# Performance work log

Hardware: AMD Instinct MI355X
Metric: run time of the kernel (lower is better)

## Reference

```python
import jax, jax.numpy as jnp
import numpy as np

XYZ_MIN = jnp.array([-1.0, -1.0, -1.0], dtype=jnp.float32)
XYZ_MAX = jnp.array([1.0, 1.0, 1.0], dtype=jnp.float32)
ALPHA_INIT = 0.01
ACT_SHIFT = float(np.log(1.0 / (1.0 - ALPHA_INIT) - 1.0))
INTERVAL = 0.5  # stepsize * voxel_size_ratio
NEAR, FAR = 0.2, 1.8
N_RAYS, N_SAMPLES = 4096, 256
GRID = 160
K0_DIM = 12
VIEW_PE = 4
WIDTH = 128
DIM0 = 3 + 3 * VIEW_PE * 2 + K0_DIM  # 39


def trilinear(grid, pts):
    """grid: [X,Y,Z,C]; pts: [N,3] world coords -> [N,C] (align_corners=True, border clamp)."""
    sz = jnp.array(grid.shape[:3], dtype=pts.dtype)
    ijk = (pts - XYZ_MIN) / (XYZ_MAX - XYZ_MIN) * (sz - 1.0)
    ijk = jnp.clip(ijk, 0.0, sz - 1.0)
    lo = jnp.clip(jnp.floor(ijk).astype(jnp.int32), 0, jnp.array(grid.shape[:3], jnp.int32) - 2)
    f = ijk - lo.astype(pts.dtype)
    hi = lo + 1
    x0, y0, z0 = lo[:, 0], lo[:, 1], lo[:, 2]
    x1, y1, z1 = hi[:, 0], hi[:, 1], hi[:, 2]
    fx, fy, fz = f[:, 0:1], f[:, 1:2], f[:, 2:3]
    c00 = grid[x0, y0, z0] * (1 - fz) + grid[x0, y0, z1] * fz
    c01 = grid[x0, y1, z0] * (1 - fz) + grid[x0, y1, z1] * fz
    c10 = grid[x1, y0, z0] * (1 - fz) + grid[x1, y0, z1] * fz
    c11 = grid[x1, y1, z0] * (1 - fz) + grid[x1, y1, z1] * fz
    c0 = c00 * (1 - fy) + c01 * fy
    c1 = c10 * (1 - fy) + c11 * fy
    return c0 * (1 - fx) + c1 * fx


def setup_inputs() -> dict:
    key = jax.random.key(0)
    ks = jax.random.split(key, 8)
    rays_o = jax.random.uniform(ks[0], (N_RAYS, 3), jnp.float32, -0.3, 0.3)
    rays_d = jax.random.normal(ks[1], (N_RAYS, 3), jnp.float32)
    density = jax.random.normal(ks[2], (GRID, GRID, GRID), jnp.float32)
    k0 = jax.random.normal(ks[3], (K0_DIM, GRID, GRID, GRID), jnp.float32) * 0.1
    W0 = jax.random.normal(ks[4], (DIM0, WIDTH), jnp.float32) * (1.0 / np.sqrt(DIM0))
    b0 = jnp.zeros((WIDTH,), jnp.float32)
    W1 = jax.random.normal(ks[5], (WIDTH, WIDTH), jnp.float32) * (1.0 / np.sqrt(WIDTH))
    b1 = jnp.zeros((WIDTH,), jnp.float32)
    W2 = jax.random.normal(ks[6], (WIDTH, 3), jnp.float32) * (1.0 / np.sqrt(WIDTH))
    b2 = jnp.zeros((3,), jnp.float32)
    return {"rays_o": rays_o, "rays_d": rays_d, "density": density, "k0": k0,
            "W0": W0, "b0": b0, "W1": W1, "b1": b1, "W2": W2, "b2": b2}


def reference(rays_o, rays_d, density, k0, W0, b0, W1, b1, W2, b2):
    R, S = rays_o.shape[0], N_SAMPLES
    viewdirs = rays_d / jnp.linalg.norm(rays_d, axis=-1, keepdims=True)
    t = jnp.linspace(NEAR, FAR, S, dtype=rays_o.dtype)  # [S]
    pts = rays_o[:, None, :] + rays_d[:, None, :] * t[None, :, None]  # [R,S,3]
    ptsf = pts.reshape(-1, 3)

    # Raw2Alpha: alpha = 1 - (1 + exp(d + shift))^(-interval)
    sigma = trilinear(density[..., None], ptsf)[:, 0].reshape(R, S)
    alpha = 1.0 - jnp.power(1.0 + jnp.exp(sigma + ACT_SHIFT), -INTERVAL)

    # Alphas2Weights: per-ray exclusive cumprod of transmittance
    Tcum = jnp.cumprod(1.0 - alpha + 1e-10, axis=1)  # [R,S]
    T = jnp.concatenate([jnp.ones((R, 1), alpha.dtype), Tcum[:, :-1]], axis=1)
    weights = alpha * T
    alphainv_last = Tcum[:, -1]

    # k0 features + view positional encoding -> rgbnet MLP
    feat = trilinear(jnp.moveaxis(k0, 0, -1), ptsf).reshape(R, S, K0_DIM)
    freq = (2.0 ** jnp.arange(VIEW_PE)).astype(rays_o.dtype)  # [P]
    vf = viewdirs[:, :, None] * freq[None, None, :]  # [R,3,P]
    vemb = jnp.concatenate([viewdirs, jnp.sin(vf).reshape(R, -1), jnp.cos(vf).reshape(R, -1)], axis=-1)  # [R,27]
    x = jnp.concatenate([feat, jnp.broadcast_to(vemb[:, None, :], (R, S, vemb.shape[-1]))], axis=-1)  # [R,S,39]

    h = jax.nn.relu(x @ W0 + b0)
    h = jax.nn.relu(h @ W1 + b1)
    rgb = jax.nn.sigmoid(h @ W2 + b2)  # [R,S,3]

    # composite with white background
    rgb_marched = jnp.sum(weights[..., None] * rgb, axis=1) + alphainv_last[:, None]
    return rgb_marched
```

## Files before the change

### kernel.cpp

```cpp
#include <hip/hip_runtime.h>
#include <hip/hip_bf16.h>

#define NRAYS 4096
#define NS 256
#define G 160
#define G2 (160*160)
#define G3 (160*160*160)
#define K0DIM 12
#define WIDTH 128
#define CHUNK 16
#define NCHUNK 16
#define HBS 136
#define ACT_SHIFT_F (-4.5951198501345889f)
#define TNEAR 0.2f
#define TFAR 1.8f

#define WS_W1G_OFF 1024
#define WS_W0G_OFF (1024 + 32768)
#define WS_PACK_OFF 65536
#define PACK_BYTES ((size_t)G3 * 16 * 2)
#define WS_NEED_AOS ((size_t)WS_PACK_OFF + PACK_BYTES)

typedef unsigned short u16;
typedef unsigned int u32;
typedef __attribute__((ext_vector_type(8))) short short8;
typedef __attribute__((ext_vector_type(4))) float floatx4;

#define W1F_IDX(kq, qs, n) (((((kq)<<2) + (qs)) * 128 + (n)) << 3)

__device__ __forceinline__ float bf2f(u16 u) {
    union { u32 i; float f; } v; v.i = ((u32)u) << 16; return v.f;
}
__device__ __forceinline__ u16 f2bf(float f) {
    union { float f; u32 u; } v; v.f = f;
    u32 r = v.u + 0x7FFFu + ((v.u >> 16) & 1u);
    return (u16)(r >> 16);
}

__device__ __forceinline__ float loadv(const float* p, int i) { return p[i]; }
__device__ __forceinline__ float loadv(const u16* p, int i)   { return bf2f(p[i]); }
__device__ __forceinline__ void storev(float* p, int i, float v) { p[i] = v; }
__device__ __forceinline__ void storev(u16* p, int i, float v)   { p[i] = f2bf(v); }
__device__ __forceinline__ float tofl(float v) { return v; }
__device__ __forceinline__ float tofl(u16 v)   { return bf2f(v); }
__device__ __forceinline__ float ldm(const void* p, int i, int mode) {
    return mode ? ((const float*)p)[i] : bf2f(((const u16*)p)[i]);
}

struct Coords { int base; float fx, fy, fz; };

__device__ __forceinline__ Coords coords_n(float px, float py, float pz) {
    float gx = fminf(fmaxf((px + 1.0f) * 79.5f, 0.0f), 159.0f);
    float gy = fminf(fmaxf((py + 1.0f) * 79.5f, 0.0f), 159.0f);
    float gz = fminf(fmaxf((pz + 1.0f) * 79.5f, 0.0f), 159.0f);
    int ix = (int)gx; if (ix > 158) ix = 158;
    int iy = (int)gy; if (iy > 158) iy = 158;
    int iz = (int)gz; if (iz > 158) iz = 158;
    Coords c;
    c.base = (ix * G + iy) * G + iz;
    c.fx = gx - (float)ix; c.fy = gy - (float)iy; c.fz = gz - (float)iz;
    return c;
}

__global__ void decide_mode(const u16* __restrict__ rays_d_u16, int* __restrict__ mode) {
    __shared__ int cnt;
    if (threadIdx.x == 0) cnt = 0;
    __syncthreads();
    if (threadIdx.x < 128) {
        u16 u = rays_d_u16[threadIdx.x];
        int e = (u >> 7) & 0xFF;
        int m = u & 0x7F;
        float v = bf2f(u);
        if (e == 0xFF || (e == 0 && m != 0) || fabsf(v) > 32.0f) atomicAdd(&cnt, 1);
    }
    __syncthreads();
    if (threadIdx.x == 0) *mode = (cnt >= 4) ? 1 : 0;
}

__global__ void pack_weights(const void* __restrict__ W1, const void* __restrict__ W0,
                             u16* __restrict__ w1g, u16* __restrict__ w0g,
                             const int* __restrict__ mode) {
    const int m = *mode;
    const int idx = blockIdx.x * 256 + threadIdx.x;
    for (int i = idx; i < WIDTH * WIDTH; i += 64 * 256) {
        int k = i >> 7, n = i & 127;
        float v = m ? ((const float*)W1)[i] : bf2f(((const u16*)W1)[i]);
        w1g[W1F_IDX(k >> 5, (k >> 3) & 3, n) + (k & 7)] = f2bf(v);
    }
    for (int i = idx; i < WIDTH * 16; i += 64 * 256) {
        int n = i >> 4, k = i & 15;
        float v = 0.0f;
        if (k < K0DIM) v = m ? ((const float*)W0)[k * WIDTH + n] : bf2f(((const u16*)W0)[k * WIDTH + n]);
        w0g[i] = f2bf(v);
    }
}

__global__ __launch_bounds__(256)
void repack_grid(const void* __restrict__ density, const void* __restrict__ k0,
                 u16* __restrict__ packed, const int* __restrict__ modep) {
    const int mode = *modep;
    const u32 vox = (u32)blockIdx.x * 128u + (u32)(threadIdx.x & 127);
    const int h = threadIdx.x >> 7;
    u16 o[8];
    if (mode) {
        const float* kf = (const float*)k0;
        const float* df = (const float*)density;
        if (h == 0) {
            #pragma unroll
            for (int c = 0; c < 8; c++) o[c] = f2bf(kf[(size_t)c*G3 + vox]);
        } else {
            #pragma unroll
            for (int c = 0; c < 4; c++) o[c] = f2bf(kf[(size_t)(8+c)*G3 + vox]);
            o[4] = f2bf(df[vox]); o[5] = 0; o[6] = 0; o[7] = 0;
        }
    } else {
        const u16* ku = (const u16*)k0;
        const u16* du = (const u16*)density;
        if (h == 0) {
            #pragma unroll
            for (int c = 0; c < 8; c++) o[c] = ku[(size_t)c*G3 + vox];
        } else {
            #pragma unroll
            for (int c = 0; c < 4; c++) o[c] = ku[(size_t)(8+c)*G3 + vox];
            o[4] = du[vox]; o[5] = 0; o[6] = 0; o[7] = 0;
        }
    }
    short8 ov;
    #pragma unroll
    for (int j = 0; j < 8; j++) ov[j] = (short)o[j];
    *(short8*)(packed + (size_t)vox*16 + (size_t)h*8) = ov;
}

__global__ __launch_bounds__(256, 4)
void dvgo_aos(const void* __restrict__ rays_o, const void* __restrict__ rays_d,
              const void* __restrict__ W0, const void* __restrict__ b0,
              const void* __restrict__ b1, const void* __restrict__ W2,
              const void* __restrict__ b2,
              const u16* __restrict__ packed, const u16* __restrict__ w1g,
              const u16* __restrict__ w0g, void* __restrict__ out,
              const int* __restrict__ modep)
{
    const int mode = *modep;

    __shared__ __align__(16) u16   featB[64 * 16];
    __shared__ __align__(16) u16   h0B[16 * HBS];
    __shared__ __align__(16) u16   h1B[16 * HBS];
    __shared__ float p2[4 * 16 * 12];
    __shared__ float rgbs[NS * 3];
    __shared__ float wts[NS];
    __shared__ float base0[WIDTH];
    __shared__ float vembs[27];
    __shared__ float ainvs;

    const int r = blockIdx.x;
    const int tid = threadIdx.x;

    const float o0 = ldm(rays_o, r*3+0, mode);
    const float o1 = ldm(rays_o, r*3+1, mode);
    const float o2 = ldm(rays_o, r*3+2, mode);
    const float d0 = ldm(rays_d, r*3+0, mode);
    const float d1 = ldm(rays_d, r*3+1, mode);
    const float d2 = ldm(rays_d, r*3+2, mode);

    const int lane = tid & 63;
    const int wvid = tid >> 6;
    const int q    = lane >> 4;
    const int ncol = lane & 15;
    const int col0 = wvid*32 + ncol;
    const int col1 = col0 + 16;

    const int sm  = tid >> 2;
    const int gdy = tid & 1;
    const int gdx = (tid >> 1) & 1;
    const u32 coff = (u32)(gdx*G2 + gdy*G) * 16u;

    float gfx, gfy, gfz;
    short8 qg[4];

    #define ISSUE_G(C0N) do {                                                     \
        float tv_ = TNEAR + (TFAR-TNEAR)*((float)((C0N)+sm) * (1.0f/255.0f));     \
        Coords ce_ = coords_n(o0+d0*tv_, o1+d1*tv_, o2+d2*tv_);                   \
        gfx = ce_.fx; gfy = ce_.fy; gfz = ce_.fz;                                 \
        const u16* g_ = packed + ((u32)ce_.base*16u + coff);                      \
        qg[0] = *(const short8*)(g_);                                             \
        qg[1] = *(const short8*)(g_ + 8);                                         \
        qg[2] = *(const short8*)(g_ + 16);                                        \
        qg[3] = *(const short8*)(g_ + 24);                                        \
    } while(0)

    #define COMMIT_G(C0N) do {                                                    \
        float wxy_ = (gdx ? gfx : 1.0f-gfx) * (gdy ? gfy : 1.0f-gfy);             \
        float v_[13];                                                             \
        _Pragma("unroll")                                                         \
        for (int c_ = 0; c_ < 8; c_++) {                                          \
            float lo_ = bf2f((u16)qg[0][c_]);                                     \
            float hi_ = bf2f((u16)qg[2][c_]);                                     \
            v_[c_] = (lo_ + gfz*(hi_-lo_)) * wxy_;                                \
        }                                                                         \
        _Pragma("unroll")                                                         \
        for (int c_ = 0; c_ < 5; c_++) {                                          \
            float lo_ = bf2f((u16)qg[1][c_]);                                     \
            float hi_ = bf2f((u16)qg[3][c_]);                                     \
            v_[8+c_] = (lo_ + gfz*(hi_-lo_)) * wxy_;                              \
        }                                                                         \
        _Pragma("unroll")                                                         \
        for (int c_ = 0; c_ < 13; c_++) {                                         \
            v_[c_] += __shfl_xor(v_[c_], 1, 64);                                  \
            v_[c_] += __shfl_xor(v_[c_], 2, 64);                                  \
        }                                                                         \
        if ((tid & 3) == 0) {                                                     \
            _Pragma("unroll")                                                     \
            for (int c_ = 0; c_ < 6; c_++) {                                      \
                u32 pk_ = (u32)f2bf(v_[2*c_]) | ((u32)f2bf(v_[2*c_+1]) << 16);    \
                *(u32*)&featB[sm*16 + 2*c_] = pk_;                                \
            }                                                                     \
            float alpha_ = 1.0f - rsqrtf(1.0f + __expf(v_[12] + ACT_SHIFT_F));    \
            wts[(C0N) + sm] = alpha_;                                             \
        }                                                                         \
    } while(0)

    ISSUE_G(0);

    short8 w1r[4][2];
    #pragma unroll
    for (int kq = 0; kq < 4; kq++) {
        w1r[kq][0] = *(const short8*)&w1g[W1F_IDX(kq, q, col0)];
        w1r[kq][1] = *(const short8*)&w1g[W1F_IDX(kq, q, col1)];
    }
    short8 w0r0 = {}, w0r1 = {};
    if (q < 2) {
        w0r0 = *(const short8*)&w0g[(col0 << 4) + q*8];
        w0r1 = *(const short8*)&w0g[(col1 << 4) + q*8];
    }
    short8 w2r;
    #pragma unroll
    for (int j = 0; j < 8; j++) {
        u16 t_ = 0;
        if (ncol < 3) t_ = f2bf(ldm(W2, (wvid*32 + q*8 + j)*3 + ncol, mode));
        w2r[j] = (short)t_;
    }
    const float b2v = (ncol < 3) ? ldm(b2, ncol, mode) : 0.0f;
    const float b1c0 = ldm(b1, col0, mode);
    const float b1c1 = ldm(b1, col1, mode);

    for (int i = tid; i < 64*4; i += 256)
        featB[(i >> 2)*16 + 12 + (i & 3)] = 0;

    if (tid < 27) {
        float inv = rsqrtf(d0*d0 + d1*d1 + d2*d2);
        float v0 = d0*inv, v1 = d1*inv, v2 = d2*inv;
        float val;
        if (tid < 3) {
            val = (tid == 0) ? v0 : ((tid == 1) ? v1 : v2);
        } else if (tid < 15) {
            int t2 = tid - 3; int dd = t2 >> 2; int p = t2 & 3;
            float vd = (dd == 0) ? v0 : ((dd == 1) ? v1 : v2);
            val = sinf(vd * (float)(1 << p));
        } else {
            int t2 = tid - 15; int dd = t2 >> 2; int p = t2 & 3;
            float vd = (dd == 0) ? v0 : ((dd == 1) ? v1 : v2);
            val = cosf(vd * (float)(1 << p));
        }
        vembs[tid] = val;
    }
    __syncthreads();

    if (tid < WIDTH) {
        float a = ldm(b0, tid, mode);
        #pragma unroll
        for (int i = 0; i < 27; i++)
            a += vembs[i] * ldm(W0, (K0DIM + i)*WIDTH + tid, mode);
        base0[tid] = a;
    }
    __syncthreads();

    const float bs00 = base0[col0], bs01 = base0[col1];

    for (int mi = 0; mi < 4; mi++) {
        COMMIT_G(mi*64);
        if (mi < 3) ISSUE_G((mi+1)*64);
        __syncthreads();

        for (int ti = 0; ti < 4; ti++) {
            short8 af0 = (short8){0,0,0,0,0,0,0,0};
            if (q < 2) af0 = *(const short8*)&featB[(ti*16 + ncol)*16 + q*8];
            floatx4 a0 = (floatx4){bs00,bs00,bs00,bs00};
            floatx4 a1 = (floatx4){bs01,bs01,bs01,bs01};
            a0 = __builtin_amdgcn_mfma_f32_16x16x32_bf16(af0, w0r0, a0, 0, 0, 0);
            a1 = __builtin_amdgcn_mfma_f32_16x16x32_bf16(af0, w0r1, a1, 0, 0, 0);
            #pragma unroll
            for (int rI = 0; rI < 4; rI++) {
                h0B[(q*4+rI)*HBS + col0] = f2bf(fmaxf(a0[rI], 0.0f));
                h0B[(q*4+rI)*HBS + col1] = f2bf(fmaxf(a1[rI], 0.0f));
            }
            __syncthreads();

            floatx4 c0a = (floatx4){b1c0,b1c0,b1c0,b1c0};
            floatx4 c1a = (floatx4){b1c1,b1c1,b1c1,b1c1};
            #pragma unroll
            for (int kq = 0; kq < 4; kq++) {
                short8 af = *(const short8*)&h0B[ncol*HBS + kq*32 + q*8];
                c0a = __builtin_amdgcn_mfma_f32_16x16x32_bf16(af, w1r[kq][0], c0a, 0, 0, 0);
                c1a = __builtin_amdgcn_mfma_f32_16x16x32_bf16(af, w1r[kq][1], c1a, 0, 0, 0);
            }
            #pragma unroll
            for (int rI = 0; rI < 4; rI++) {
                h1B[(q*4+rI)*HBS + col0] = f2bf(fmaxf(c0a[rI], 0.0f));
                h1B[(q*4+rI)*HBS + col1] = f2bf(fmaxf(c1a[rI], 0.0f));
            }
            __syncthreads();

            short8 af2 = *(const short8*)&h1B[ncol*HBS + wvid*32 + q*8];
            floatx4 pp = (floatx4){0.0f,0.0f,0.0f,0.0f};
            if (wvid == 0 && ncol < 3) pp = (floatx4){b2v,b2v,b2v,b2v};
            pp = __builtin_amdgcn_mfma_f32_16x16x32_bf16(af2, w2r, pp, 0, 0, 0);
            if (ncol < 3) {
                #pragma unroll
                for (int rI = 0; rI < 4; rI++)
                    p2[ti*192 + (q*4+rI)*12 + wvid*3 + ncol] = pp[rI];
            }
            __syncthreads();

            if (tid < 48) {
                int c_ = tid >> 4, s_ = tid & 15;
                int pb = ti*192 + s_*12;
                float x = p2[pb + c_] + p2[pb + 3 + c_] + p2[pb + 6 + c_] + p2[pb + 9 + c_];
                rgbs[(mi*64 + ti*16 + s_)*3 + c_] = 1.0f / (1.0f + __expf(-x));
            }
        }
    }

    __syncthreads();

    if (tid < 64) {
        const int l = tid;
        float a0 = wts[4*l+0], a1 = wts[4*l+1], a2 = wts[4*l+2], a3 = wts[4*l+3];
        float m0 = 1.0f - a0 + 1e-10f;
        float m1 = 1.0f - a1 + 1e-10f;
        float m2 = 1.0f - a2 + 1e-10f;
        float m3 = 1.0f - a3 + 1e-10f;
        float sc = (m0*m1)*(m2*m3);
        #pragma unroll
        for (int dlt = 1; dlt < 64; dlt <<= 1) {
            float o = __shfl_up(sc, dlt, 64);
            if (l >= dlt) sc *= o;
        }
        float Tr = __shfl_up(sc, 1, 64);
        if (l == 0) Tr = 1.0f;
        wts[4*l+0] = a0 * Tr; Tr *= m0;
        wts[4*l+1] = a1 * Tr; Tr *= m1;
        wts[4*l+2] = a2 * Tr; Tr *= m2;
        wts[4*l+3] = a3 * Tr; Tr *= m3;
        if (l == 63) ainvs = Tr;
    }
    __syncthreads();

    if (wvid < 3) {
        float a = 0.0f;
        #pragma unroll
        for (int j = 0; j < 4; j++) {
            int s = lane*4 + j;
            a += wts[s] * rgbs[s*3 + wvid];
        }
        #pragma unroll
        for (int m = 1; m <= 32; m <<= 1) a += __shfl_xor(a, m, 64);
        if (lane == 0) {
            float v = a + ainvs;
            if (mode) ((float*)out)[r*3 + wvid] = v;
            else      ((u16*)out)[r*3 + wvid]   = f2bf(v);
        }
    }
    #undef ISSUE_G
    #undef COMMIT_G
}

template <typename T, typename OT, int MODE>
__global__ __launch_bounds__(256, 4)
void dvgo_fb(const T* __restrict__ rays_o, const T* __restrict__ rays_d,
             const T* __restrict__ density, const T* __restrict__ k0,
             const T* __restrict__ W0, const T* __restrict__ b0,
             const T* __restrict__ W1, const T* __restrict__ b1,
             const T* __restrict__ W2, const T* __restrict__ b2,
             const u16* __restrict__ w1g, const u16* __restrict__ w0g,
             OT* __restrict__ out, const int* __restrict__ mode)
{
    if (*mode != MODE) return;

    __shared__ __align__(16) u16   h0B[CHUNK * HBS];
    __shared__ __align__(16) u16   featB[CHUNK * 16];
    __shared__ __align__(16) float W2Tf[3 * WIDTH];
    __shared__ float p2[CHUNK * 12];
    __shared__ float base0[WIDTH];
    __shared__ float b1s[WIDTH];
    __shared__ float b2s[3];
    __shared__ float vembs[27];
    __shared__ float wts[NS];
    __shared__ float red[48];
    __shared__ float ainvs;

    const int r = blockIdx.x;
    const int tid = threadIdx.x;

    const float o0 = loadv(rays_o, r*3+0);
    const float o1 = loadv(rays_o, r*3+1);
    const float o2 = loadv(rays_o, r*3+2);
    const float d0 = loadv(rays_d, r*3+0);
    const float d1 = loadv(rays_d, r*3+1);
    const float d2 = loadv(rays_d, r*3+2);

    const int lane = tid & 63;
    const int wvid = tid >> 6;
    const int q    = lane >> 4;
    const int ncol = lane & 15;
    const int col0 = wvid*32 + ncol;
    const int col1 = col0 + 16;

    T areg[8]; float afx, afy, afz;
    {
        float tv = TNEAR + (TFAR - TNEAR) * ((float)tid * (1.0f/(float)(NS-1)));
        Coords c = coords_n(o0 + d0*tv, o1 + d1*tv, o2 + d2*tv);
        afx = c.fx; afy = c.fy; afz = c.fz;
        const T* g = density + (u32)c.base;
        areg[0]=g[0]; areg[1]=g[1]; areg[2]=g[G]; areg[3]=g[G+1];
        areg[4]=g[G2]; areg[5]=g[G2+1]; areg[6]=g[G2+G]; areg[7]=g[G2+G+1];
    }

    short8 w1r[4][2];
    #pragma unroll
    for (int kq = 0; kq < 4; kq++) {
        w1r[kq][0] = *(const short8*)&w1g[W1F_IDX(kq, q, col0)];
        w1r[kq][1] = *(const short8*)&w1g[W1F_IDX(kq, q, col1)];
    }
    short8 w0r0 = {}, w0r1 = {};
    if (q < 2) {
        w0r0 = *(const short8*)&w0g[(col0 << 4) + q*8];
        w0r1 = *(const short8*)&w0g[(col1 << 4) + q*8];
    }

    const int gch = tid >> 4;
    const int gs  = tid & 15;
    const bool gact = (gch < K0DIM);
    const T* gbase = k0 + (size_t)(gact ? gch : 0) * G3;

    #define ISSUE(C0N, Q, FX, FY, FZ) do { if (gact) {                          \
        float tv_ = TNEAR + (TFAR-TNEAR)*((float)((C0N)+gs) * (1.0f/255.0f));   \
        Coords ce_ = coords_n(o0+d0*tv_, o1+d1*tv_, o2+d2*tv_);                 \
        FX = ce_.fx; FY = ce_.fy; FZ = ce_.fz;                                  \
        const T* g_ = gbase + (u32)ce_.base;                                    \
        Q[0]=g_[0]; Q[1]=g_[1]; Q[2]=g_[G]; Q[3]=g_[G+1];                       \
        Q[4]=g_[G2]; Q[5]=g_[G2+1]; Q[6]=g_[G2+G]; Q[7]=g_[G2+G+1];             \
    } } while(0)

    #define COMMIT(Q, FX, FY, FZ) do { if (gact) {                              \
        float z0_=tofl(Q[0]), z1_=tofl(Q[1]), z2_=tofl(Q[2]), z3_=tofl(Q[3]);   \
        float z4_=tofl(Q[4]), z5_=tofl(Q[5]), z6_=tofl(Q[6]), z7_=tofl(Q[7]);   \
        float c00_ = z0_ + (FZ)*(z1_-z0_);                                      \
        float c01_ = z2_ + (FZ)*(z3_-z2_);                                      \
        float c10_ = z4_ + (FZ)*(z5_-z4_);                                      \
        float c11_ = z6_ + (FZ)*(z7_-z6_);                                      \
        float e0_ = c00_ + (FY)*(c01_-c00_);                                    \
        float e1_ = c10_ + (FY)*(c11_-c10_);                                    \
        featB[gs*16 + gch] = f2bf(e0_ + (FX)*(e1_-e0_));                        \
    } } while(0)

    T qa[8], qn[8];
    float fxa, fya, fza, fxn, fyn, fzn;
    ISSUE(0, qa, fxa, fya, fza);
    ISSUE(CHUNK, qn, fxn, fyn, fzn);

    for (int i = tid; i < CHUNK*4; i += 256)
        featB[(i >> 2)*16 + 12 + (i & 3)] = 0;
    for (int k = tid; k < 3*WIDTH; k += 256) {
        int c = k >> 7, i = k & 127;
        W2Tf[k] = loadv(W2, i*3 + c);
    }
    if (tid < WIDTH) b1s[tid] = loadv(b1, tid);
    if (tid < 3)     b2s[tid] = loadv(b2, tid);

    if (tid < 27) {
        float inv = rsqrtf(d0*d0 + d1*d1 + d2*d2);
        float v0 = d0*inv, v1 = d1*inv, v2 = d2*inv;
        float val;
        if (tid < 3) {
            val = (tid == 0) ? v0 : ((tid == 1) ? v1 : v2);
        } else if (tid < 15) {
            int t2 = tid - 3; int dd = t2 >> 2; int p = t2 & 3;
            float vd = (dd == 0) ? v0 : ((dd == 1) ? v1 : v2);
            val = sinf(vd * (float)(1 << p));
        } else {
            int t2 = tid - 15; int dd = t2 >> 2; int p = t2 & 3;
            float vd = (dd == 0) ? v0 : ((dd == 1) ? v1 : v2);
            val = cosf(vd * (float)(1 << p));
        }
        vembs[tid] = val;
    }
    __syncthreads();

    if (tid < WIDTH) {
        float a = loadv(b0, tid);
        #pragma unroll
        for (int i = 0; i < 27; i++)
            a += vembs[i] * loadv(W0, (K0DIM + i)*WIDTH + tid);
        base0[tid] = a;
    }

    {
        float z0=tofl(areg[0]), z1=tofl(areg[1]), z2=tofl(areg[2]), z3=tofl(areg[3]);
        float z4=tofl(areg[4]), z5=tofl(areg[5]), z6=tofl(areg[6]), z7=tofl(areg[7]);
        float c00 = z0 + afz*(z1-z0);
        float c01 = z2 + afz*(z3-z2);
        float c10 = z4 + afz*(z5-z4);
        float c11 = z6 + afz*(z7-z6);
        float e0 = c00 + afy*(c01-c00);
        float e1 = c10 + afy*(c11-c10);
        float sigma = e0 + afx*(e1-e0);
        float alpha = 1.0f - rsqrtf(1.0f + __expf(sigma + ACT_SHIFT_F));
        wts[tid] = alpha;
    }
    __syncthreads();

    if (tid < 64) {
        const int l = tid;
        float a0 = wts[4*l+0], a1 = wts[4*l+1], a2 = wts[4*l+2], a3 = wts[4*l+3];
        float m0 = 1.0f - a0 + 1e-10f;
        float m1 = 1.0f - a1 + 1e-10f;
        float m2 = 1.0f - a2 + 1e-10f;
        float m3 = 1.0f - a3 + 1e-10f;
        float sc = (m0*m1)*(m2*m3);
        #pragma unroll
        for (int dlt = 1; dlt < 64; dlt <<= 1) {
            float o = __shfl_up(sc, dlt, 64);
            if (l >= dlt) sc *= o;
        }
        float Tr = __shfl_up(sc, 1, 64);
        if (l == 0) Tr = 1.0f;
        wts[4*l+0] = a0 * Tr; Tr *= m0;
        wts[4*l+1] = a1 * Tr; Tr *= m1;
        wts[4*l+2] = a2 * Tr; Tr *= m2;
        wts[4*l+3] = a3 * Tr; Tr *= m3;
        if (l == 63) ainvs = Tr;
    }
    __syncthreads();

    const float bs00 = base0[col0], bs01 = base0[col1];
    const float b1c0 = b1s[col0],   b1c1 = b1s[col1];
    const float w200 = W2Tf[col0], w210 = W2Tf[WIDTH+col0], w220 = W2Tf[2*WIDTH+col0];
    const float w201 = W2Tf[col1], w211 = W2Tf[WIDTH+col1], w221 = W2Tf[2*WIDTH+col1];

    float rgbacc = 0.0f;

    #define CHUNK_BODY(Q, FX, FY, FZ, CI) do {                                       \
        COMMIT(Q, FX, FY, FZ);                                                       \
        __syncthreads();                                                             \
        {                                                                            \
            short8 af0 = (short8){0,0,0,0,0,0,0,0};                                  \
            if (q < 2) af0 = *(const short8*)&featB[ncol*16 + q*8];                  \
            floatx4 a0_ = (floatx4){bs00, bs00, bs00, bs00};                         \
            floatx4 a1_ = (floatx4){bs01, bs01, bs01, bs01};                         \
            a0_ = __builtin_amdgcn_mfma_f32_16x16x32_bf16(af0, w0r0, a0_, 0, 0, 0);  \
            a1_ = __builtin_amdgcn_mfma_f32_16x16x32_bf16(af0, w0r1, a1_, 0, 0, 0);  \
            _Pragma("unroll")                                                        \
            for (int rI = 0; rI < 4; rI++) {                                         \
                h0B[(q*4+rI)*HBS + col0] = f2bf(fmaxf(a0_[rI], 0.0f));               \
                h0B[(q*4+rI)*HBS + col1] = f2bf(fmaxf(a1_[rI], 0.0f));               \
            }                                                                        \
        }                                                                            \
        __syncthreads();                                                             \
        if ((CI) + 2 < NCHUNK) ISSUE(((CI)+2)*CHUNK, Q, FX, FY, FZ);                 \
        {                                                                            \
            floatx4 a0_ = (floatx4){b1c0, b1c0, b1c0, b1c0};                         \
            floatx4 a1_ = (floatx4){b1c1, b1c1, b1c1, b1c1};                         \
            _Pragma("unroll")                                                        \
            for (int kq = 0; kq < 4; kq++) {                                         \
                short8 af_ = *(const short8*)&h0B[ncol*HBS + kq*32 + q*8];           \
                a0_ = __builtin_amdgcn_mfma_f32_16x16x32_bf16(af_, w1r[kq][0], a0_, 0, 0, 0); \
                a1_ = __builtin_amdgcn_mfma_f32_16x16x32_bf16(af_, w1r[kq][1], a1_, 0, 0, 0); \
            }                                                                        \
            float p_[3][4];                                                          \
            _Pragma("unroll")                                                        \
            for (int rI = 0; rI < 4; rI++) {                                         \
                float h0_ = fmaxf(a0_[rI], 0.0f);                                    \
                float h1_ = fmaxf(a1_[rI], 0.0f);                                    \
                p_[0][rI] = h0_*w200 + h1_*w201;                                     \
                p_[1][rI] = h0_*w210 + h1_*w211;                                     \
                p_[2][rI] = h0_*w220 + h1_*w221;                                     \
            }                                                                        \
            _Pragma("unroll")                                                        \
            for (int m_ = 1; m_ <= 8; m_ <<= 1) {                                    \
                _Pragma("unroll")                                                    \
                for (int c_ = 0; c_ < 3; c_++) {                                     \
                    _Pragma("unroll")                                                \
                    for (int rI = 0; rI < 4; rI++)                                   \
                        p_[c_][rI] += __shfl_xor(p_[c_][rI], m_, 64);                \
                }                                                                    \
            }                                                                        \
            if (ncol == 0) {                                                         \
                _Pragma("unroll")                                                    \
                for (int rI = 0; rI < 4; rI++) {                                     \
                    _Pragma("unroll")                                                \
                    for (int c_ = 0; c_ < 3; c_++)                                   \
                        p2[(q*4+rI)*12 + wvid*3 + c_] = p_[c_][rI];                  \
                }                                                                    \
            }                                                                        \
        }                                                                            \
        __syncthreads();                                                             \
        if (tid < 48) {                                                              \
            int c_ = tid >> 4, s_ = tid & 15;                                        \
            float x_ = b2s[c_] + p2[s_*12 + c_] + p2[s_*12 + 3 + c_]                 \
                     + p2[s_*12 + 6 + c_] + p2[s_*12 + 9 + c_];                      \
            float rgb_ = 1.0f / (1.0f + __expf(-x_));                                \
            rgbacc += wts[(CI)*CHUNK + s_] * rgb_;                                   \
        }                                                                            \
    } while(0)

    for (int cc = 0; cc < NCHUNK; cc += 2) {
        CHUNK_BODY(qa, fxa, fya, fza, cc);
        CHUNK_BODY(qn, fxn, fyn, fzn, cc + 1);
    }

    if (tid < 48) red[tid] = rgbacc;
    __syncthreads();
    if (tid < 3) {
        float s = 0.0f;
        #pragma unroll
        for (int k = 0; k < 16; k++) s += red[tid*16 + k];
        storev(out, r*3 + tid, s + ainvs);
    }
    #undef ISSUE
    #undef COMMIT
    #undef CHUNK_BODY
}

extern "C" void kernel_launch(void* const* d_in, const int* in_sizes, int n_in,
                              void* d_out, int out_size, void* d_ws, size_t ws_size,
                              hipStream_t stream) {
    int* mode = (int*)d_ws;
    u16* w1g = (u16*)((char*)d_ws + WS_W1G_OFF);
    u16* w0g = (u16*)((char*)d_ws + WS_W0G_OFF);

    decide_mode<<<dim3(1), dim3(128), 0, stream>>>((const u16*)d_in[1], mode);
    pack_weights<<<dim3(64), dim3(256), 0, stream>>>(d_in[6], d_in[4], w1g, w0g, mode);

    if (ws_size >= WS_NEED_AOS) {
        u16* packed = (u16*)((char*)d_ws + WS_PACK_OFF);
        repack_grid<<<dim3(G3/128), dim3(256), 0, stream>>>(d_in[2], d_in[3], packed, mode);
        dvgo_aos<<<dim3(NRAYS), dim3(256), 0, stream>>>(
            d_in[0], d_in[1], d_in[4], d_in[5], d_in[7], d_in[8], d_in[9],
            packed, w1g, w0g, d_out, mode);
    } else {
        dvgo_fb<u16, u16, 0><<<dim3(NRAYS), dim3(256), 0, stream>>>(
            (const u16*)d_in[0], (const u16*)d_in[1], (const u16*)d_in[2],
            (const u16*)d_in[3], (const u16*)d_in[4], (const u16*)d_in[5],
            (const u16*)d_in[6], (const u16*)d_in[7], (const u16*)d_in[8],
            (const u16*)d_in[9], w1g, w0g, (u16*)d_out, mode);
        dvgo_fb<float, float, 1><<<dim3(NRAYS), dim3(256), 0, stream>>>(
            (const float*)d_in[0], (const float*)d_in[1], (const float*)d_in[2],
            (const float*)d_in[3], (const float*)d_in[4], (const float*)d_in[5],
            (const float*)d_in[6], (const float*)d_in[7], (const float*)d_in[8],
            (const float*)d_in[9], w1g, w0g, (float*)d_out, mode);
    }
}
```

Measured before the change: 479.1 us.

## Batch MLP layers across 64 samples, fold output layer into shuffles, vectorize grid repack

```diff
diff --git a/kernel.cpp b/kernel.cpp
--- a/kernel.cpp
+++ b/kernel.cpp
@@ -99,36 +99,38 @@
 void repack_grid(const void* __restrict__ density, const void* __restrict__ k0,
                  u16* __restrict__ packed, const int* __restrict__ modep) {
     const int mode = *modep;
-    const u32 vox = (u32)blockIdx.x * 128u + (u32)(threadIdx.x & 127);
-    const int h = threadIdx.x >> 7;
-    u16 o[8];
+    const u32 v0 = ((u32)blockIdx.x * 256u + (u32)threadIdx.x) * 2u;
+    u16 a[13], b[13];
     if (mode) {
         const float* kf = (const float*)k0;
-        const float* df = (const float*)density;
-        if (h == 0) {
-            #pragma unroll
-            for (int c = 0; c < 8; c++) o[c] = f2bf(kf[(size_t)c*G3 + vox]);
-        } else {
-            #pragma unroll
-            for (int c = 0; c < 4; c++) o[c] = f2bf(kf[(size_t)(8+c)*G3 + vox]);
-            o[4] = f2bf(df[vox]); o[5] = 0; o[6] = 0; o[7] = 0;
-        }
+        #pragma unroll
+        for (int c = 0; c < 12; c++) {
+            float2 t = *(const float2*)(kf + (size_t)c*G3 + v0);
+            a[c] = f2bf(t.x); b[c] = f2bf(t.y);
+        }
+        float2 d = *(const float2*)((const float*)density + v0);
+        a[12] = f2bf(d.x); b[12] = f2bf(d.y);
     } else {
         const u16* ku = (const u16*)k0;
-        const u16* du = (const u16*)density;
-        if (h == 0) {
-            #pragma unroll
-            for (int c = 0; c < 8; c++) o[c] = ku[(size_t)c*G3 + vox];
-        } else {
-            #pragma unroll
-            for (int c = 0; c < 4; c++) o[c] = ku[(size_t)(8+c)*G3 + vox];
-            o[4] = du[vox]; o[5] = 0; o[6] = 0; o[7] = 0;
-        }
-    }
-    short8 ov;
+        #pragma unroll
+        for (int c = 0; c < 12; c++) {
+            u32 t = *(const u32*)(ku + (size_t)c*G3 + v0);
+            a[c] = (u16)t; b[c] = (u16)(t >> 16);
+        }
+        u32 d = *(const u32*)((const u16*)density + v0);
+        a[12] = (u16)d; b[12] = (u16)(d >> 16);
+    }
+    short8 o0v, o1v, o2v, o3v;
     #pragma unroll
-    for (int j = 0; j < 8; j++) ov[j] = (short)o[j];
-    *(short8*)(packed + (size_t)vox*16 + (size_t)h*8) = ov;
+    for (int j = 0; j < 8; j++) { o0v[j] = (short)a[j]; o2v[j] = (short)b[j]; }
+    #pragma unroll
+    for (int j = 0; j < 5; j++) { o1v[j] = (short)a[8+j]; o3v[j] = (short)b[8+j]; }
+    o1v[5]=0; o1v[6]=0; o1v[7]=0; o3v[5]=0; o3v[6]=0; o3v[7]=0;
+    u16* p = packed + (size_t)v0 * 16;
+    *(short8*)(p)      = o0v;
+    *(short8*)(p + 8)  = o1v;
+    *(short8*)(p + 16) = o2v;
+    *(short8*)(p + 24) = o3v;
 }
 
 __global__ __launch_bounds__(256, 4)
@@ -143,13 +145,13 @@
     const int mode = *modep;
 
     __shared__ __align__(16) u16   featB[64 * 16];
-    __shared__ __align__(16) u16   h0B[16 * HBS];
-    __shared__ __align__(16) u16   h1B[16 * HBS];
+    __shared__ __align__(16) u16   h0B[64 * HBS];
     __shared__ float p2[4 * 16 * 12];
     __shared__ float rgbs[NS * 3];
     __shared__ float wts[NS];
     __shared__ float base0[WIDTH];
     __shared__ float vembs[27];
+    __shared__ float b2s[3];
     __shared__ float ainvs;
 
     const int r = blockIdx.x;
@@ -232,19 +234,14 @@
         w0r0 = *(const short8*)&w0g[(col0 << 4) + q*8];
         w0r1 = *(const short8*)&w0g[(col1 << 4) + q*8];
     }
-    short8 w2r;
-    #pragma unroll
-    for (int j = 0; j < 8; j++) {
-        u16 t_ = 0;
-        if (ncol < 3) t_ = f2bf(ldm(W2, (wvid*32 + q*8 + j)*3 + ncol, mode));
-        w2r[j] = (short)t_;
-    }
-    const float b2v = (ncol < 3) ? ldm(b2, ncol, mode) : 0.0f;
+    const float w200 = ldm(W2, col0*3+0, mode), w210 = ldm(W2, col0*3+1, mode), w220 = ldm(W2, col0*3+2, mode);
+    const float w201 = ldm(W2, col1*3+0, mode), w211 = ldm(W2, col1*3+1, mode), w221 = ldm(W2, col1*3+2, mode);
     const float b1c0 = ldm(b1, col0, mode);
     const float b1c1 = ldm(b1, col1, mode);
 
     for (int i = tid; i < 64*4; i += 256)
         featB[(i >> 2)*16 + 12 + (i & 3)] = 0;
+    if (tid < 3) b2s[tid] = ldm(b2, tid, mode);
 
     if (tid < 27) {
         float inv = rsqrtf(d0*d0 + d1*d1 + d2*d2);
@@ -281,52 +278,66 @@
         if (mi < 3) ISSUE_G((mi+1)*64);
         __syncthreads();
 
-        for (int ti = 0; ti < 4; ti++) {
+        #pragma unroll
+        for (int mt = 0; mt < 4; mt++) {
             short8 af0 = (short8){0,0,0,0,0,0,0,0};
-            if (q < 2) af0 = *(const short8*)&featB[(ti*16 + ncol)*16 + q*8];
+            if (q < 2) af0 = *(const short8*)&featB[(mt*16 + ncol)*16 + q*8];
             floatx4 a0 = (floatx4){bs00,bs00,bs00,bs00};
             floatx4 a1 = (floatx4){bs01,bs01,bs01,bs01};
             a0 = __builtin_amdgcn_mfma_f32_16x16x32_bf16(af0, w0r0, a0, 0, 0, 0);
             a1 = __builtin_amdgcn_mfma_f32_16x16x32_bf16(af0, w0r1, a1, 0, 0, 0);
             #pragma unroll
             for (int rI = 0; rI < 4; rI++) {
-                h0B[(q*4+rI)*HBS + col0] = f2bf(fmaxf(a0[rI], 0.0f));
-                h0B[(q*4+rI)*HBS + col1] = f2bf(fmaxf(a1[rI], 0.0f));
+                h0B[(mt*16 + q*4 + rI)*HBS + col0] = f2bf(fmaxf(a0[rI], 0.0f));
+                h0B[(mt*16 + q*4 + rI)*HBS + col1] = f2bf(fmaxf(a1[rI], 0.0f));
             }
-            __syncthreads();
-
+        }
+        __syncthreads();
+
+        #pragma unroll 2
+        for (int mt = 0; mt < 4; mt++) {
             floatx4 c0a = (floatx4){b1c0,b1c0,b1c0,b1c0};
             floatx4 c1a = (floatx4){b1c1,b1c1,b1c1,b1c1};
             #pragma unroll
             for (int kq = 0; kq < 4; kq++) {
-                short8 af = *(const short8*)&h0B[ncol*HBS + kq*32 + q*8];
+                short8 af = *(const short8*)&h0B[(mt*16 + ncol)*HBS + kq*32 + q*8];
                 c0a = __builtin_amdgcn_mfma_f32_16x16x32_bf16(af, w1r[kq][0], c0a, 0, 0, 0);
                 c1a = __builtin_amdgcn_mfma_f32_16x16x32_bf16(af, w1r[kq][1], c1a, 0, 0, 0);
             }
+            float p_[3][4];
             #pragma unroll
             for (int rI = 0; rI < 4; rI++) {
-                h1B[(q*4+rI)*HBS + col0] = f2bf(fmaxf(c0a[rI], 0.0f));
-                h1B[(q*4+rI)*HBS + col1] = f2bf(fmaxf(c1a[rI], 0.0f));
+                float h0_ = fmaxf(c0a[rI], 0.0f);
+                float h1_ = fmaxf(c1a[rI], 0.0f);
+                p_[0][rI] = h0_*w200 + h1_*w201;
+                p_[1][rI] = h0_*w210 + h1_*w211;
+                p_[2][rI] = h0_*w220 + h1_*w221;
             }
-            __syncthreads();
-
-            short8 af2 = *(const short8*)&h1B[ncol*HBS + wvid*32 + q*8];
-            floatx4 pp = (floatx4){0.0f,0.0f,0.0f,0.0f};
-            if (wvid == 0 && ncol < 3) pp = (floatx4){b2v,b2v,b2v,b2v};
-            pp = __builtin_amdgcn_mfma_f32_16x16x32_bf16(af2, w2r, pp, 0, 0, 0);
-            if (ncol < 3) {
+            #pragma unroll
+            for (int m_ = 1; m_ <= 8; m_ <<= 1) {
                 #pragma unroll
-                for (int rI = 0; rI < 4; rI++)
-                    p2[ti*192 + (q*4+rI)*12 + wvid*3 + ncol] = pp[rI];
+                for (int c_ = 0; c_ < 3; c_++) {
+                    #pragma unroll
+                    for (int rI = 0; rI < 4; rI++)
+                        p_[c_][rI] += __shfl_xor(p_[c_][rI], m_, 64);
+                }
             }
-            __syncthreads();
-
-            if (tid < 48) {
-                int c_ = tid >> 4, s_ = tid & 15;
-                int pb = ti*192 + s_*12;
-                float x = p2[pb + c_] + p2[pb + 3 + c_] + p2[pb + 6 + c_] + p2[pb + 9 + c_];
-                rgbs[(mi*64 + ti*16 + s_)*3 + c_] = 1.0f / (1.0f + __expf(-x));
+            if (ncol == 0) {
+                #pragma unroll
+                for (int rI = 0; rI < 4; rI++) {
+                    #pragma unroll
+                    for (int c_ = 0; c_ < 3; c_++)
+                        p2[mt*192 + (q*4+rI)*12 + wvid*3 + c_] = p_[c_][rI];
+                }
             }
+        }
+        __syncthreads();
+
+        if (tid < 192) {
+            int c_ = tid >> 6, s_ = tid & 63;
+            int pb = (s_ >> 4)*192 + (s_ & 15)*12 + c_;
+            float x = b2s[c_] + p2[pb] + p2[pb+3] + p2[pb+6] + p2[pb+9];
+            rgbs[(mi*64 + s_)*3 + c_] = 1.0f / (1.0f + __expf(-x));
         }
     }
 
@@ -643,7 +654,7 @@
 
     if (ws_size >= WS_NEED_AOS) {
         u16* packed = (u16*)((char*)d_ws + WS_PACK_OFF);
-        repack_grid<<<dim3(G3/128), dim3(256), 0, stream>>>(d_in[2], d_in[3], packed, mode);
+        repack_grid<<<dim3(G3/512), dim3(256), 0, stream>>>(d_in[2], d_in[3], packed, mode);
         dvgo_aos<<<dim3(NRAYS), dim3(256), 0, stream>>>(
             d_in[0], d_in[1], d_in[4], d_in[5], d_in[7], d_in[8], d_in[9],
             packed, w1g, w0g, d_out, mode);
```

New measurement: 555.2 us. 15.9% more time.
